# Kernel optimization log

Measured on AMD Instinct MI355X. Metric: run time of the kernel, lower is better.

The kernel has to match this reference:

```python
import jax, jax.numpy as jnp
import numpy as np

B, LAT, HC, HD, NB, S, E, NOTES = 64, 512, 1024, 1024, 16, 16, 128, 128
OUT = NOTES * 3  # 128 pitches x 3 states
L = 2            # num LSTM layers


def setup_inputs() -> dict:
    key = jax.random.key(0)
    ks = jax.random.split(key, 16)
    def w(k, *shape):
        return jax.random.normal(k, shape, jnp.float32) * 0.02
    G, GD = 4 * HC, 4 * HD
    z32 = lambda *s: jnp.zeros(s, jnp.float32)
    return {
        "z": jax.random.normal(ks[0], (B, LAT), jnp.float32),
        "target_pianoroll": jax.random.randint(ks[1], (B, NB * S, NOTES), 0, 3, jnp.int32),
        "w_zc": w(ks[2], HC * L * 2, LAT), "b_zc": z32(HC * L * 2),
        "c_wih0": w(ks[3], G, 1),  "c_whh0": w(ks[4], G, HC), "c_bih0": z32(G), "c_bhh0": z32(G),
        "c_wih1": w(ks[5], G, HC), "c_whh1": w(ks[6], G, HC), "c_bih1": z32(G), "c_bhh1": z32(G),
        "np_w": w(ks[7], E, NOTES), "np_b": z32(E),
        "cd_w": w(ks[8], HD * L * 2, HC), "cd_b": z32(HD * L * 2),
        "d_wih0": w(ks[9], GD, HC + E), "d_whh0": w(ks[10], GD, HD), "d_bih0": z32(GD), "d_bhh0": z32(GD),
        "d_wih1": w(ks[11], GD, HD),    "d_whh1": w(ks[12], GD, HD), "d_bih1": z32(GD), "d_bhh1": z32(GD),
        "op_w": w(ks[13], OUT, HD), "op_b": z32(OUT),
    }


def _lstm_cell(x, h, c, wih, whh, bih, bhh):
    g = x @ wih.T + h @ whh.T + (bih + bhh)
    i, f, gg, o = jnp.split(g, 4, axis=-1)  # PyTorch gate order i,f,g,o
    c = jax.nn.sigmoid(f) * c + jax.nn.sigmoid(i) * jnp.tanh(gg)
    h = jax.nn.sigmoid(o) * jnp.tanh(c)
    return h, c


def _run_lstm2(xs, h0, c0, p0, p1):
    # xs: [T, Bm, D]; h0/c0: [2, Bm, H]; returns [T, Bm, H] (top-layer outputs)
    def step(carry, xt):
        h0l, c0l, h1l, c1l = carry
        h0l, c0l = _lstm_cell(xt, h0l, c0l, *p0)
        h1l, c1l = _lstm_cell(h0l, h1l, c1l, *p1)
        return (h0l, c0l, h1l, c1l), h1l
    _, ys = jax.lax.scan(step, (h0[0], c0[0], h0[1], c0[1]), xs)
    return ys


def _forward(z, target_pianoroll, w_zc, b_zc,
             c_wih0, c_whh0, c_bih0, c_bhh0, c_wih1, c_whh1, c_bih1, c_bhh1,
             np_w, np_b, cd_w, cd_b,
             d_wih0, d_whh0, d_bih0, d_bhh0, d_wih1, d_whh1, d_bih1, d_bhh1,
             op_w, op_b):
    b = z.shape[0]
    # z -> conductor initial (h, c): view(B,2,L,HC).permute(2,0,3,1)
    ini = (z @ w_zc.T + b_zc).reshape(b, 2, L, HC)
    h_c0 = jnp.transpose(ini[:, 0], (1, 0, 2))  # [L, B, HC]
    c_c0 = jnp.transpose(ini[:, 1], (1, 0, 2))
    # Conductor LSTM over num_bars of zero inputs
    cond_xs = jnp.zeros((NB, b, 1), z.dtype)
    cond = _run_lstm2(cond_xs, h_c0, c_c0,
                      (c_wih0, c_whh0, c_bih0, c_bhh0),
                      (c_wih1, c_whh1, c_bih1, c_bhh1))  # [NB, B, HC]
    # Per-bar decoder initial states -> fold bars into batch ([L, NB*B, HD])
    di = (cond @ cd_w.T + cd_b).reshape(NB, b, 2, L, HD)
    h_d0 = jnp.transpose(di[:, :, 0], (2, 0, 1, 3)).reshape(L, NB * b, HD)
    c_d0 = jnp.transpose(di[:, :, 1], (2, 0, 1, 3)).reshape(L, NB * b, HD)
    # Teacher-forced prev inputs: zeros at t=0, shifted target otherwise
    tf = target_pianoroll.astype(z.dtype)                       # [B, NB*S, 128]
    prev = jnp.concatenate([jnp.zeros((b, 1, NOTES), z.dtype), tf[:, :-1]], axis=1)
    prev = jnp.transpose(prev.reshape(b, NB, S, NOTES), (2, 1, 0, 3)).reshape(S, NB * b, NOTES)
    emb = prev @ np_w.T + np_b                                   # [S, NB*B, E]
    bar = jnp.broadcast_to(cond.reshape(NB * b, HC), (S, NB * b, HC))
    xs = jnp.concatenate([emb, bar], axis=-1)                    # [S, NB*B, E+HC]
    ys = _run_lstm2(xs, h_d0, c_d0,
                    (d_wih0, d_whh0, d_bih0, d_bhh0),
                    (d_wih1, d_whh1, d_bih1, d_bhh1))            # [S, NB*B, HD]
    logits = ys @ op_w.T + op_b                                  # [S, NB*B, 384]
    logits = jnp.transpose(logits.reshape(S, NB, b, OUT), (2, 1, 0, 3))
    return logits.reshape(b, NB * S, NOTES, 3)


def reference(z, target_pianoroll, w_zc, b_zc,
              c_wih0, c_whh0, c_bih0, c_bhh0, c_wih1, c_whh1, c_bih1, c_bhh1,
              np_w, np_b, cd_w, cd_b,
              d_wih0, d_whh0, d_bih0, d_bhh0, d_wih1, d_whh1, d_bih1, d_bhh1,
              op_w, op_b):
    return _forward(z, target_pianoroll, w_zc, b_zc,
                    c_wih0, c_whh0, c_bih0, c_bhh0, c_wih1, c_whh1, c_bih1, c_bhh1,
                    np_w, np_b, cd_w, cd_b,
                    d_wih0, d_whh0, d_bih0, d_bhh0, d_wih1, d_whh1, d_bih1, d_bhh1,
                    op_w, op_b)
```

## Files before the change

### kernel.cpp

```cpp
#include <hip/hip_runtime.h>
#include <math.h>


typedef __attribute__((ext_vector_type(8))) short s16x8;
typedef __attribute__((ext_vector_type(8))) _Float16 f16x8;
typedef __attribute__((ext_vector_type(4))) float f32x4;

__device__ inline unsigned short f2h(float f) {
    _Float16 h = (_Float16)f;
    return __builtin_bit_cast(unsigned short, h);
}
__device__ inline float h2f(unsigned short u) {
    _Float16 h = __builtin_bit_cast(_Float16, u);
    return (float)h;
}

__device__ __forceinline__ void gload16(const unsigned short* g, char* l) {
    const unsigned int* gu = (const unsigned int*)g;
    unsigned int* lu = (unsigned int*)l;
    __builtin_amdgcn_global_load_lds(
        (const __attribute__((address_space(1))) unsigned int*)gu,
        (__attribute__((address_space(3))) unsigned int*)lu, 16, 0, 0);
}

__global__ __launch_bounds__(256) void gemm_mfma(
    int M, int N,
    const unsigned short* __restrict__ A1h, const unsigned short* __restrict__ A1l, int K1, int lda1,
    const unsigned short* __restrict__ W1h, int ldw1,
    const unsigned short* __restrict__ A2h, const unsigned short* __restrict__ A2l, int K2, int lda2,
    const unsigned short* __restrict__ W2h, int ldw2,
    const float* __restrict__ Add, int ldadd,
    const float* __restrict__ b1, const float* __restrict__ b2,
    float* __restrict__ C, int ldc,
    unsigned short* __restrict__ Chi, unsigned short* __restrict__ Clo,
    unsigned short* __restrict__ cpyh, unsigned short* __restrict__ cpyl,
    int mode, int scatter_s)
{
    __shared__ __align__(16) char ldsb[49152];

    const int tid = threadIdx.x;
    const int lane = tid & 63;
    const int wv = tid >> 6;
    const int wm = wv >> 1;
    const int wn = wv & 1;

    const int gx = gridDim.x;
    const int l = blockIdx.y * gx + blockIdx.x;
    const int nwg = gx * gridDim.y;
    const int l2 = (l & 7) * (nwg >> 3) + (l >> 3);
    const int bm = (l2 % gx) * 64;
    const int bn = (l2 / gx) * 128;

    const int j = (lane & 7) ^ (lane >> 3);
    const bool isLo = j >= 4;
    const int koff = (j & 3) * 8;
    const int rsub = lane >> 3;
    const int aR0 = bm + wv * 8 + rsub;
    const int brs = lane >> 2;
    const int j2 = (lane & 3) ^ ((lane >> 3) & 3);
    const int koffB = j2 * 8;

    f32x4 acc[2][4];
#pragma unroll
    for (int m = 0; m < 2; ++m)
#pragma unroll
        for (int n = 0; n < 4; ++n) acc[m][n] = (f32x4)0.0f;

    const int fr = lane & 15;
    const int kc = lane >> 4;

    const int NT = (K1 + K2) >> 5;

#define STAGE(dstp, t) {                                                        \
        const int k0_ = (t) << 5;                                               \
        const bool ph2_ = (k0_ >= K1);                                          \
        const unsigned short* Ab_ = ph2_ ? (isLo ? A2l : A2h)                   \
                                         : (isLo ? A1l : A1h);                  \
        const unsigned short* Wb_ = ph2_ ? W2h : W1h;                           \
        const int lda_ = ph2_ ? lda2 : lda1;                                    \
        const int ldw_ = ph2_ ? ldw2 : ldw1;                                    \
        const int kb_ = ph2_ ? (k0_ - K1) : k0_;                                \
        char* dst_ = (dstp);                                                    \
        gload16(Ab_ + (size_t)aR0 * lda_ + kb_ + koff,        dst_ + (wv    ) * 1024); \
        gload16(Ab_ + (size_t)(aR0 + 32) * lda_ + kb_ + koff, dst_ + (wv + 4) * 1024); \
        gload16(Wb_ + (size_t)(bn + wv * 16 + brs) * ldw_ + kb_ + koffB,        \
                dst_ + 8192 + wv * 1024);                                       \
        gload16(Wb_ + (size_t)(bn + 64 + wv * 16 + brs) * ldw_ + kb_ + koffB,   \
                dst_ + 8192 + 4096 + wv * 1024);                                \
    }

    char* bcur  = ldsb;
    char* bnext = ldsb + 16384;
    char* bfar  = ldsb + 32768;

    STAGE(bcur, 0);
    STAGE(bnext, 1);
    asm volatile("s_waitcnt vmcnt(4)" ::: "memory");
    __builtin_amdgcn_s_barrier();

    for (int t = 0; t < NT; ++t) {
        const bool more = (t + 2 < NT);
        if (more) STAGE(bfar, t + 2);
        {
            f16x8 ah[2], al[2], bh[4];
#pragma unroll
            for (int m = 0; m < 2; ++m) {
                const int row = wm * 32 + m * 16 + fr;
                const int sw = (row & 7) << 4;
                char* base = bcur + row * 128;
                ah[m] = *(const f16x8*)(base + ((kc * 16) ^ sw));
                al[m] = *(const f16x8*)(base + (((kc + 4) * 16) ^ sw));
            }
#pragma unroll
            for (int n = 0; n < 4; ++n) {
                const int brow = wn * 64 + n * 16 + fr;
                bh[n] = *(const f16x8*)(bcur + 8192 + brow * 64 +
                                        ((kc ^ ((brow >> 1) & 3)) << 4));
            }
            __builtin_amdgcn_s_setprio(1);
#pragma unroll
            for (int m = 0; m < 2; ++m)
#pragma unroll
                for (int n = 0; n < 4; ++n) {
                    acc[m][n] = __builtin_amdgcn_mfma_f32_16x16x32_f16(ah[m], bh[n], acc[m][n], 0, 0, 0);
                    acc[m][n] = __builtin_amdgcn_mfma_f32_16x16x32_f16(al[m], bh[n], acc[m][n], 0, 0, 0);
                }
            __builtin_amdgcn_s_setprio(0);
        }
        if (more) { asm volatile("s_waitcnt vmcnt(4)" ::: "memory"); }
        else      { asm volatile("s_waitcnt vmcnt(0)" ::: "memory"); }
        __builtin_amdgcn_s_barrier();
        char* tmp = bcur; bcur = bnext; bnext = bfar; bfar = tmp;
    }
#undef STAGE

    if (mode == 4) {
        float* ldsf = (float*)ldsb;
#pragma unroll
        for (int m = 0; m < 2; ++m)
#pragma unroll
            for (int n = 0; n < 4; ++n) {
                f32x4 v4 = acc[m][n];
#pragma unroll
                for (int q = 0; q < 4; ++q) {
                    const int rl = wm * 32 + m * 16 + kc * 4 + q;
                    const int cl = wn * 64 + n * 16 + fr;
                    const int col = bn + cl;
                    float v = v4[q];
                    if (b1) v += b1[col];
                    if (Add) v += Add[(size_t)(bm + rl) * ldadd + col];
                    ldsf[rl * 132 + cl] = v;
                }
            }
        __syncthreads();
        const int kb = bn >> 2;
#pragma unroll
        for (int e = 0; e < 8; ++e) {
            const int idx2 = tid * 8 + e;
            const int row = idx2 >> 5, kk = idx2 & 31;
            const float4 g4 = *(const float4*)(ldsf + row * 132 + kk * 4);
            const size_t ci = (((size_t)(bm + row)) << 10) + kb + kk;
            const float si = 1.f / (1.f + expf(-g4.x));
            const float sf = 1.f / (1.f + expf(-g4.y));
            const float so = 1.f / (1.f + expf(-g4.w));
            const float cn = sf * C[ci] + si * tanhf(g4.z);
            const float hn = so * tanhf(cn);
            C[ci] = cn;
            const unsigned short hh = f2h(hn);
            const unsigned short hl = f2h(hn - h2f(hh));
            Chi[ci] = hh; Clo[ci] = hl;
            if (cpyh) { cpyh[ci] = hh; cpyl[ci] = hl; }
        }
        return;
    }

#pragma unroll
    for (int m = 0; m < 2; ++m)
#pragma unroll
        for (int n = 0; n < 4; ++n) {
            f32x4 v4 = acc[m][n];
#pragma unroll
            for (int q = 0; q < 4; ++q) {
                const int rl = wm * 32 + m * 16 + kc * 4 + q;
                const int cl = wn * 64 + n * 16 + fr;
                const int r = bm + rl, col = bn + cl;
                float v = v4[q];
                if (b1) v += b1[col];
                if (b2) v += b2[col];
                if (Add) v += Add[(size_t)r * ldadd + col];
                if (mode == 0) {
                    C[(size_t)r * ldc + col] = v;
                } else if (mode == 1) {
                    unsigned short h = f2h(v);
                    Chi[(size_t)r * ldc + col] = h;
                    Clo[(size_t)r * ldc + col] = f2h(v - h2f(h));
                } else if (mode == 2) {
                    const int bb = r & 63, nb = r >> 6;
                    C[(size_t)(((bb * 16 + nb) * 16 + scatter_s)) * 384 + col] = v;
                } else {
                    const int bb = r & 63, nb = (r >> 6) & 15, s = r >> 10;
                    C[(size_t)(((bb * 16 + nb) * 16 + s)) * 384 + col] = v;
                }
            }
        }
}

__global__ __launch_bounds__(256) void gemm_mfma_n64(
    int M, int N,
    const unsigned short* __restrict__ A1h, const unsigned short* __restrict__ A1l, int K1, int lda1,
    const unsigned short* __restrict__ W1h, int ldw1,
    const unsigned short* __restrict__ A2h, const unsigned short* __restrict__ A2l, int K2, int lda2,
    const unsigned short* __restrict__ W2h, int ldw2,
    const float* __restrict__ b1,
    float* __restrict__ C, int ldc,
    unsigned short* __restrict__ Chi, unsigned short* __restrict__ Clo,
    unsigned short* __restrict__ cpyh, unsigned short* __restrict__ cpyl,
    int mode)
{
    __shared__ __align__(16) char ldsb[36864];

    const int tid = threadIdx.x;
    const int lane = tid & 63;
    const int wv = tid >> 6;

    const int gx = gridDim.x;
    const int l = blockIdx.y * gx + blockIdx.x;
    const int nwg = gx * gridDim.y;
    const int l2 = (l & 7) * (nwg >> 3) + (l >> 3);
    const int bm = (l2 % gx) * 64;
    const int bn = (l2 / gx) * 64;

    const int j = (lane & 7) ^ (lane >> 3);
    const bool isLo = j >= 4;
    const int koff = (j & 3) * 8;
    const int rsub = lane >> 3;
    const int aR0 = bm + wv * 8 + rsub;
    const int brs = lane >> 2;
    const int j2 = (lane & 3) ^ ((lane >> 3) & 3);
    const int koffB = j2 * 8;

    f32x4 acc[4];
#pragma unroll
    for (int m = 0; m < 4; ++m) acc[m] = (f32x4)0.0f;

    const int fr = lane & 15;
    const int kc = lane >> 4;

    const int NT = (K1 + K2) >> 5;

#define STAGE64(dstp, t) {                                                      \
        const int k0_ = (t) << 5;                                               \
        const bool ph2_ = (k0_ >= K1);                                          \
        const unsigned short* Ab_ = ph2_ ? (isLo ? A2l : A2h)                   \
                                         : (isLo ? A1l : A1h);                  \
        const unsigned short* Wb_ = ph2_ ? W2h : W1h;                           \
        const int lda_ = ph2_ ? lda2 : lda1;                                    \
        const int ldw_ = ph2_ ? ldw2 : ldw1;                                    \
        const int kb_ = ph2_ ? (k0_ - K1) : k0_;                                \
        char* dst_ = (dstp);                                                    \
        gload16(Ab_ + (size_t)aR0 * lda_ + kb_ + koff,        dst_ + (wv    ) * 1024); \
        gload16(Ab_ + (size_t)(aR0 + 32) * lda_ + kb_ + koff, dst_ + (wv + 4) * 1024); \
        gload16(Wb_ + (size_t)(bn + wv * 16 + brs) * ldw_ + kb_ + koffB,        \
                dst_ + 8192 + wv * 1024);                                       \
    }

    char* bcur  = ldsb;
    char* bnext = ldsb + 12288;
    char* bfar  = ldsb + 24576;

    STAGE64(bcur, 0);
    STAGE64(bnext, 1);
    asm volatile("s_waitcnt vmcnt(3)" ::: "memory");
    __builtin_amdgcn_s_barrier();

    for (int t = 0; t < NT; ++t) {
        const bool more = (t + 2 < NT);
        if (more) STAGE64(bfar, t + 2);
        {
            f16x8 ah[4], al[4], bh;
#pragma unroll
            for (int m = 0; m < 4; ++m) {
                const int row = m * 16 + fr;
                const int sw = (row & 7) << 4;
                char* base = bcur + row * 128;
                ah[m] = *(const f16x8*)(base + ((kc * 16) ^ sw));
                al[m] = *(const f16x8*)(base + (((kc + 4) * 16) ^ sw));
            }
            {
                const int brow = wv * 16 + fr;
                bh = *(const f16x8*)(bcur + 8192 + brow * 64 +
                                     ((kc ^ ((brow >> 1) & 3)) << 4));
            }
            __builtin_amdgcn_s_setprio(1);
#pragma unroll
            for (int m = 0; m < 4; ++m) {
                acc[m] = __builtin_amdgcn_mfma_f32_16x16x32_f16(ah[m], bh, acc[m], 0, 0, 0);
                acc[m] = __builtin_amdgcn_mfma_f32_16x16x32_f16(al[m], bh, acc[m], 0, 0, 0);
            }
            __builtin_amdgcn_s_setprio(0);
        }
        if (more) { asm volatile("s_waitcnt vmcnt(3)" ::: "memory"); }
        else      { asm volatile("s_waitcnt vmcnt(0)" ::: "memory"); }
        __builtin_amdgcn_s_barrier();
        char* tmp = bcur; bcur = bnext; bnext = bfar; bfar = tmp;
    }
#undef STAGE64

    if (mode == 4) {
        float* ldsf = (float*)ldsb;
#pragma unroll
        for (int m = 0; m < 4; ++m) {
            f32x4 v4 = acc[m];
#pragma unroll
            for (int q = 0; q < 4; ++q) {
                const int rl = m * 16 + kc * 4 + q;
                const int cl = wv * 16 + fr;
                float v = v4[q];
                if (b1) v += b1[bn + cl];
                ldsf[rl * 68 + cl] = v;
            }
        }
        __syncthreads();
        const int kb = bn >> 2;
#pragma unroll
        for (int e = 0; e < 4; ++e) {
            const int idx2 = tid * 4 + e;
            const int row = idx2 >> 4, kk = idx2 & 15;
            const float4 g4 = *(const float4*)(ldsf + row * 68 + kk * 4);
            const size_t ci = (((size_t)(bm + row)) << 10) + kb + kk;
            const float si = 1.f / (1.f + expf(-g4.x));
            const float sf = 1.f / (1.f + expf(-g4.y));
            const float so = 1.f / (1.f + expf(-g4.w));
            const float cn = sf * C[ci] + si * tanhf(g4.z);
            const float hn = so * tanhf(cn);
            C[ci] = cn;
            const unsigned short hh = f2h(hn);
            const unsigned short hl = f2h(hn - h2f(hh));
            Chi[ci] = hh; Clo[ci] = hl;
            if (cpyh) { cpyh[ci] = hh; cpyl[ci] = hl; }
        }
        return;
    }

#pragma unroll
    for (int m = 0; m < 4; ++m) {
        f32x4 v4 = acc[m];
#pragma unroll
        for (int q = 0; q < 4; ++q) {
            const int rl = m * 16 + kc * 4 + q;
            const int cl = wv * 16 + fr;
            const int r = bm + rl, col = bn + cl;
            float v = v4[q];
            if (b1) v += b1[col];
            C[(size_t)r * ldc + col] = v;
        }
    }
}

__global__ __launch_bounds__(256) void split_pack(
    const float* __restrict__ src, int ldsrc, int c0, long total, int C,
    unsigned short* __restrict__ hi, unsigned short* __restrict__ lo)
{
    long i = ((long)blockIdx.x * 256 + threadIdx.x) * 4;
    if (i >= total) return;
    int r = (int)(i / C), c = (int)(i % C);
    float4 v = *(const float4*)(src + (size_t)r * ldsrc + c0 + c);
#pragma unroll
    for (int j = 0; j < 4; ++j) {
        float x = (&v.x)[j];
        unsigned short h = f2h(x);
        hi[i + j] = h;
        lo[i + j] = f2h(x - h2f(h));
    }
}

__global__ __launch_bounds__(256) void split_pack_perm(
    const float* __restrict__ src, int ldsrc, int c0, long total, int C,
    unsigned short* __restrict__ hi, unsigned short* __restrict__ lo)
{
    long i = ((long)blockIdx.x * 256 + threadIdx.x) * 4;
    if (i >= total) return;
    int r = (int)(i / C), c = (int)(i % C);
    int sr = (r & 3) * 1024 + (r >> 2);
    float4 v = *(const float4*)(src + (size_t)sr * ldsrc + c0 + c);
#pragma unroll
    for (int j = 0; j < 4; ++j) {
        float x = (&v.x)[j];
        unsigned short h = f2h(x);
        hi[i + j] = h;
        lo[i + j] = f2h(x - h2f(h));
    }
}

__global__ __launch_bounds__(256) void bias_perm(
    const float* __restrict__ a, const float* __restrict__ b, float* __restrict__ dst)
{
    const int j = blockIdx.x * 256 + threadIdx.x;
    if (j >= 4096) return;
    const int o = (j & 3) * 1024 + (j >> 2);
    dst[j] = a[o] + b[o];
}

__global__ __launch_bounds__(256) void scatter_ini_split(
    const float* __restrict__ I, unsigned short* __restrict__ hchi,
    unsigned short* __restrict__ hclo, float* __restrict__ cc)
{
    const int idx = blockIdx.x * blockDim.x + threadIdx.x;
    if (idx >= 131072) return;
    const int k = idx & 1023, b = (idx >> 10) & 63, l = idx >> 16;
    const float* row = I + (size_t)b * 4096;
    float hv = row[(l << 10) + k];
    unsigned short h = f2h(hv);
    hchi[idx] = h; hclo[idx] = f2h(hv - h2f(h));
    cc[idx] = row[2048 + (l << 10) + k];
}

__global__ __launch_bounds__(256) void scatter_di_split(
    const float* __restrict__ D,
    unsigned short* __restrict__ h0h, unsigned short* __restrict__ h0l,
    unsigned short* __restrict__ h1h, unsigned short* __restrict__ h1l,
    float* __restrict__ cd0, float* __restrict__ cd1)
{
    const int idx = blockIdx.x * blockDim.x + threadIdx.x;
    if (idx >= 1048576) return;
    const int k = idx & 1023, r = idx >> 10;
    const float* row = D + ((size_t)r << 12);
    float v0 = row[k], v1 = row[1024 + k];
    unsigned short a = f2h(v0); h0h[idx] = a; h0l[idx] = f2h(v0 - h2f(a));
    unsigned short b = f2h(v1); h1h[idx] = b; h1l[idx] = f2h(v1 - h2f(b));
    cd0[idx] = row[2048 + k];
    cd1[idx] = row[3072 + k];
}

__global__ __launch_bounds__(256) void build_prev_b(
    const int* __restrict__ tp, unsigned short* __restrict__ ph, unsigned short* __restrict__ pl)
{
    const int idx = blockIdx.x * blockDim.x + threadIdx.x;
    if (idx >= 2097152) return;
    const int n = idx & 127;
    const int r = (idx >> 7) & 1023;
    const int s = idx >> 17;
    const int nb = r >> 6, bb = r & 63;
    const int t = nb * 16 + s;
    float v = 0.f;
    if (t > 0) v = (float)tp[(size_t)bb * 32768 + (size_t)(t - 1) * 128 + n];
    ph[idx] = f2h(v);
    pl[idx] = 0;
}

#define BM 64
#define BN 64
#define BK 16

__global__ __launch_bounds__(256) void gemm_f32(
    int M, int N,
    const float* __restrict__ A1, int K1, int lda1,
    const float* __restrict__ W1, int ldw1,
    const float* __restrict__ A2, int K2, int lda2,
    const float* __restrict__ W2, int ldw2,
    const float* __restrict__ Add, int ldadd,
    const float* __restrict__ bias1, const float* __restrict__ bias2,
    float* __restrict__ C, int ldc, int scatter_s)
{
    __shared__ float As[BK][BM];
    __shared__ float Ws[BK][BN];
    const int bm = blockIdx.x * BM;
    const int bn = blockIdx.y * BN;
    const int tid = threadIdx.x;
    const int ty = tid >> 4;
    const int tx = tid & 15;
    const int lr = tid >> 2;
    const int lc = (tid & 3) << 2;

    float acc[4][4] = {{0.f,0.f,0.f,0.f},{0.f,0.f,0.f,0.f},{0.f,0.f,0.f,0.f},{0.f,0.f,0.f,0.f}};

    for (int phase = 0; phase < 2; ++phase) {
        const float* Ap = phase ? A2 : A1;
        const float* Wp = phase ? W2 : W1;
        const int K   = phase ? K2 : K1;
        const int lda = phase ? lda2 : lda1;
        const int ldw = phase ? ldw2 : ldw1;
        if (Ap == nullptr || K <= 0) continue;
        for (int k0 = 0; k0 < K; k0 += BK) {
            float4 av = *(const float4*)(Ap + (size_t)(bm + lr) * lda + k0 + lc);
            float4 wv = *(const float4*)(Wp + (size_t)(bn + lr) * ldw + k0 + lc);
            __syncthreads();
            As[lc+0][lr] = av.x; As[lc+1][lr] = av.y; As[lc+2][lr] = av.z; As[lc+3][lr] = av.w;
            Ws[lc+0][lr] = wv.x; Ws[lc+1][lr] = wv.y; Ws[lc+2][lr] = wv.z; Ws[lc+3][lr] = wv.w;
            __syncthreads();
            #pragma unroll
            for (int k = 0; k < BK; ++k) {
                float4 a = *(const float4*)&As[k][ty << 2];
                float4 w = *(const float4*)&Ws[k][tx << 2];
                acc[0][0] = fmaf(a.x, w.x, acc[0][0]);
                acc[0][1] = fmaf(a.x, w.y, acc[0][1]);
                acc[0][2] = fmaf(a.x, w.z, acc[0][2]);
                acc[0][3] = fmaf(a.x, w.w, acc[0][3]);
                acc[1][0] = fmaf(a.y, w.x, acc[1][0]);
                acc[1][1] = fmaf(a.y, w.y, acc[1][1]);
                acc[1][2] = fmaf(a.y, w.z, acc[1][2]);
                acc[1][3] = fmaf(a.y, w.w, acc[1][3]);
                acc[2][0] = fmaf(a.z, w.x, acc[2][0]);
                acc[2][1] = fmaf(a.z, w.y, acc[2][1]);
                acc[2][2] = fmaf(a.z, w.z, acc[2][2]);
                acc[2][3] = fmaf(a.z, w.w, acc[2][3]);
                acc[3][0] = fmaf(a.w, w.x, acc[3][0]);
                acc[3][1] = fmaf(a.w, w.y, acc[3][1]);
                acc[3][2] = fmaf(a.w, w.z, acc[3][2]);
                acc[3][3] = fmaf(a.w, w.w, acc[3][3]);
            }
        }
    }

    #pragma unroll
    for (int i = 0; i < 4; ++i) {
        const int row = bm + (ty << 2) + i;
        #pragma unroll
        for (int j = 0; j < 4; ++j) {
            const int col = bn + (tx << 2) + j;
            float v = acc[i][j];
            if (bias1) v += bias1[col];
            if (bias2) v += bias2[col];
            if (Add)   v += Add[(size_t)row * ldadd + col];
            if (scatter_s >= 0) {
                const int bb = row & 63, nb = row >> 6;
                C[(size_t)(((bb * 16 + nb) * 16 + scatter_s)) * 384 + col] = v;
            } else {
                C[(size_t)row * ldc + col] = v;
            }
        }
    }
}

__global__ __launch_bounds__(256) void lstm_cell(
    const float* __restrict__ g, float* __restrict__ c,
    float* __restrict__ h, float* __restrict__ hcopy, int M)
{
    const int idx = blockIdx.x * blockDim.x + threadIdx.x;
    if (idx >= (M << 10)) return;
    const int r = idx >> 10, k = idx & 1023;
    const float* gr = g + ((size_t)r << 12);
    const float gi = gr[k], gf = gr[k + 1024], gg = gr[k + 2048], go = gr[k + 3072];
    const float si = 1.f / (1.f + expf(-gi));
    const float sf = 1.f / (1.f + expf(-gf));
    const float so = 1.f / (1.f + expf(-go));
    const float cn = sf * c[idx] + si * tanhf(gg);
    const float hn = so * tanhf(cn);
    c[idx] = cn;
    h[idx] = hn;
    if (hcopy) hcopy[idx] = hn;
}

__global__ __launch_bounds__(256) void scatter_ini(
    const float* __restrict__ I, float* __restrict__ hc, float* __restrict__ cc)
{
    const int idx = blockIdx.x * blockDim.x + threadIdx.x;
    if (idx >= 131072) return;
    const int k = idx & 1023, b = (idx >> 10) & 63, l = idx >> 16;
    const float* row = I + (size_t)b * 4096;
    hc[idx] = row[(l << 10) + k];
    cc[idx] = row[2048 + (l << 10) + k];
}

__global__ __launch_bounds__(256) void scatter_di(
    const float* __restrict__ D, float* __restrict__ hd0, float* __restrict__ cd0,
    float* __restrict__ hd1, float* __restrict__ cd1)
{
    const int idx = blockIdx.x * blockDim.x + threadIdx.x;
    if (idx >= 1048576) return;
    const int k = idx & 1023, r = idx >> 10;
    const float* row = D + ((size_t)r << 12);
    hd0[idx] = row[k];
    hd1[idx] = row[1024 + k];
    cd0[idx] = row[2048 + k];
    cd1[idx] = row[3072 + k];
}

__global__ __launch_bounds__(256) void build_prev(
    const int* __restrict__ tp, float* __restrict__ prevf)
{
    const int idx = blockIdx.x * blockDim.x + threadIdx.x;
    if (idx >= 2097152) return;
    const int n = idx & 127;
    const int r = (idx >> 7) & 1023;
    const int s = idx >> 17;
    const int nb = r >> 6, bb = r & 63;
    const int t = nb * 16 + s;
    float v = 0.f;
    if (t > 0) v = (float)tp[(size_t)bb * 32768 + (size_t)(t - 1) * 128 + n];
    prevf[idx] = v;
}

extern "C" void kernel_launch(void* const* d_in, const int* in_sizes, int n_in,
                              void* d_out, int out_size, void* d_ws, size_t ws_size,
                              hipStream_t stream)
{
    (void)in_sizes; (void)n_in; (void)out_size;
    const float* z      = (const float*)d_in[0];
    const int*   tp     = (const int*)  d_in[1];
    const float* w_zc   = (const float*)d_in[2];
    const float* b_zc   = (const float*)d_in[3];
    const float* c_whh0 = (const float*)d_in[5];
    const float* c_bih0 = (const float*)d_in[6];
    const float* c_bhh0 = (const float*)d_in[7];
    const float* c_wih1 = (const float*)d_in[8];
    const float* c_whh1 = (const float*)d_in[9];
    const float* c_bih1 = (const float*)d_in[10];
    const float* c_bhh1 = (const float*)d_in[11];
    const float* np_w   = (const float*)d_in[12];
    const float* np_b   = (const float*)d_in[13];
    const float* cd_w   = (const float*)d_in[14];
    const float* cd_b   = (const float*)d_in[15];
    const float* d_wih0 = (const float*)d_in[16];
    const float* d_whh0 = (const float*)d_in[17];
    const float* d_bih0 = (const float*)d_in[18];
    const float* d_bhh0 = (const float*)d_in[19];
    const float* d_wih1 = (const float*)d_in[20];
    const float* d_whh1 = (const float*)d_in[21];
    const float* d_bih1 = (const float*)d_in[22];
    const float* d_bhh1 = (const float*)d_in[23];
    const float* op_w   = (const float*)d_in[24];
    const float* op_b   = (const float*)d_in[25];
    float* out = (float*)d_out;

    size_t o = 0;
    auto alloc = [&](size_t bytes) { size_t r = o; o = (o + bytes + 255) & ~(size_t)255; return r; };
    const size_t oCW0 = alloc((size_t)4096*1024*4);
    const size_t oCW1 = alloc((size_t)4096*1024*4);
    const size_t oCW2 = alloc((size_t)4096*1024*4);
    const size_t oWZC = alloc((size_t)4096*512*4);
    const size_t oNPW = alloc((size_t)128*128*4);
    const size_t oZS  = alloc((size_t)64*512*4);
    const size_t oCDW = alloc((size_t)4096*1024*4);
    const size_t oD0R = alloc((size_t)4096*1024*4);
    const size_t oCG  = alloc((size_t)64*4096*4);
    const size_t oCC  = alloc((size_t)2*64*1024*4);
    const size_t oHCa = alloc((size_t)2*64*1024*4);
    const size_t oHCb = alloc((size_t)2*64*1024*4);
    const size_t oCND = alloc((size_t)1024*1024*4);
    const size_t oEMB = alloc((size_t)16*1024*128*4);
    const size_t oBRP = alloc((size_t)1024*4096*4);
    const size_t oDG  = alloc((size_t)1024*4096*4);
    const size_t oHD0a= alloc((size_t)1024*1024*4);
    const size_t oHD0b= alloc((size_t)1024*1024*4);
    const size_t oHD1a= alloc((size_t)1024*1024*4);
    const size_t oHD1b= alloc((size_t)1024*1024*4);
    const size_t oCD0 = alloc((size_t)1024*1024*4);
    const size_t oCD1 = alloc((size_t)1024*1024*4);
    const size_t oBS  = alloc((size_t)4*4096*4);
    const size_t need = o;
    const size_t oH1S = alloc((size_t)16*1024*1024*4);
    const size_t need_batched = o;

    if (ws_size >= need) {
        const bool batched = (ws_size >= need_batched);
        char* ws = (char*)d_ws;
        unsigned short* CW0 = (unsigned short*)(ws + oCW0);
        unsigned short* CW1 = (unsigned short*)(ws + oCW1);
        unsigned short* CW2 = (unsigned short*)(ws + oCW2);
        unsigned short* WZC = (unsigned short*)(ws + oWZC);
        unsigned short* NPW = (unsigned short*)(ws + oNPW);
        unsigned short* ZS  = (unsigned short*)(ws + oZS);
        unsigned short* CDW = (unsigned short*)(ws + oCDW);
        unsigned short* D0R = (unsigned short*)(ws + oD0R);
        float* CG  = (float*)(ws + oCG);
        float* CC  = (float*)(ws + oCC);
        unsigned short* HCa = (unsigned short*)(ws + oHCa);
        unsigned short* HCb = (unsigned short*)(ws + oHCb);
        unsigned short* CND = (unsigned short*)(ws + oCND);
        unsigned short* PRV = (unsigned short*)(ws + oDG);
        unsigned short* EMB = (unsigned short*)(ws + oEMB);
        float* BRP = (float*)(ws + oBRP);
        float* DG  = (float*)(ws + oDG);
        unsigned short* HD0a = (unsigned short*)(ws + oHD0a);
        unsigned short* HD0b = (unsigned short*)(ws + oHD0b);
        unsigned short* HD1a = (unsigned short*)(ws + oHD1a);
        unsigned short* HD1b = (unsigned short*)(ws + oHD1b);
        float* CD0 = (float*)(ws + oCD0);
        float* CD1 = (float*)(ws + oCD1);
        float* BSC0 = (float*)(ws + oBS);
        float* BSC1 = BSC0 + 4096;
        float* BSB0 = BSC1 + 4096;
        float* BSD1 = BSB0 + 4096;
        unsigned short* H1S  = (unsigned short*)(ws + oH1S);
        unsigned short* H1Sl = H1S + (size_t)16*1048576;
        unsigned short* DWHH0 = CW0;
        unsigned short* DWIH1 = CW1;
        unsigned short* DWHH1 = CW2;
        unsigned short* D0E   = WZC;
        unsigned short* OPW   = WZC + (size_t)2*4096*128;

        auto split = [&](const float* src, int ldsrc, int c0, long R, long C, unsigned short* dst) {
            long total = R * C;
            split_pack<<<(unsigned)((total/4 + 255) / 256), 256, 0, stream>>>(
                src, ldsrc, c0, total, (int)C, dst, dst + total);
        };
        auto splitP = [&](const float* src, int ldsrc, int c0, long C, unsigned short* dst) {
            long total = 4096 * C;
            split_pack_perm<<<(unsigned)((total/4 + 255) / 256), 256, 0, stream>>>(
                src, ldsrc, c0, total, (int)C, dst, dst + total);
        };
        auto gemm2 = [&](int M, int N,
                         const unsigned short* A1h, const unsigned short* A1l, int K1, int lda1,
                         const unsigned short* W1, int ldw1,
                         const unsigned short* A2h, const unsigned short* A2l, int K2, int lda2,
                         const unsigned short* W2, int ldw2,
                         const float* Addp, int ldadd, const float* bb1, const float* bb2,
                         float* Cp, int ldc, unsigned short* Chi, unsigned short* Clo,
                         unsigned short* cpyh, unsigned short* cpyl,
                         int mode, int ss) {
            dim3 grid(M / 64, N / 128);
            gemm_mfma<<<grid, 256, 0, stream>>>(M, N, A1h, A1l, K1, lda1, W1, ldw1,
                                                A2h, A2l, K2, lda2, W2, ldw2,
                                                Addp, ldadd, bb1, bb2, Cp, ldc, Chi, Clo,
                                                cpyh, cpyl, mode, ss);
        };
        auto gemmN64 = [&](int M, int N,
                           const unsigned short* A1h, const unsigned short* A1l, int K1, int lda1,
                           const unsigned short* W1, int ldw1,
                           const unsigned short* A2h, const unsigned short* A2l, int K2, int lda2,
                           const unsigned short* W2, int ldw2,
                           const float* bb1, float* Cp, int ldc,
                           unsigned short* Chi, unsigned short* Clo,
                           unsigned short* cpyh, unsigned short* cpyl, int mode) {
            dim3 grid(M / 64, N / 64);
            gemm_mfma_n64<<<grid, 256, 0, stream>>>(M, N, A1h, A1l, K1, lda1, W1, ldw1,
                                                    A2h, A2l, K2, lda2, W2, ldw2,
                                                    bb1, Cp, ldc, Chi, Clo, cpyh, cpyl, mode);
        };

        auto hc0h = [&](int b){ return (b ? HCb : HCa); };
        auto hc0l = [&](int b){ return (b ? HCb : HCa) + 131072; };
        auto hc1h = [&](int b){ return (b ? HCb : HCa) + 65536; };
        auto hc1l = [&](int b){ return (b ? HCb : HCa) + 131072 + 65536; };
        auto hd0h = [&](int b){ return (b ? HD0b : HD0a); };
        auto hd0l = [&](int b){ return (b ? HD0b : HD0a) + 1048576; };
        auto hd1h = [&](int b){ return (b ? HD1b : HD1a); };
        auto hd1l = [&](int b){ return (b ? HD1b : HD1a) + 1048576; };

        split(z, 512, 0, 64, 512, ZS);
        split(w_zc, 512, 0, 4096, 512, WZC);
        splitP(c_whh0, 1024, 0, 1024, CW0);
        splitP(c_wih1, 1024, 0, 1024, CW1);
        splitP(c_whh1, 1024, 0, 1024, CW2);
        split(np_w, 128, 0, 128, 128, NPW);
        split(cd_w, 1024, 0, 4096, 1024, CDW);
        splitP(d_wih0, 1152, 128, 1024, D0R);
        bias_perm<<<16, 256, 0, stream>>>(c_bih0, c_bhh0, BSC0);
        bias_perm<<<16, 256, 0, stream>>>(c_bih1, c_bhh1, BSC1);
        bias_perm<<<16, 256, 0, stream>>>(d_bih0, d_bhh0, BSB0);
        bias_perm<<<16, 256, 0, stream>>>(d_bih1, d_bhh1, BSD1);
        build_prev_b<<<8192, 256, 0, stream>>>(tp, PRV, PRV + 2097152);

        gemmN64(64, 4096, ZS, ZS + 32768, 512, 512, WZC, 512,
                nullptr, nullptr, 0, 0, nullptr, 0,
                b_zc, CG, 4096, nullptr, nullptr, nullptr, nullptr, 0);
        scatter_ini_split<<<512, 256, 0, stream>>>(CG, HCa, HCa + 131072, CC);

        gemm2(16384, 128, PRV, PRV + 2097152, 128, 128, NPW, 128,
              nullptr, nullptr, 0, 0, nullptr, 0,
              nullptr, 0, np_b, nullptr, nullptr, 128, EMB, EMB + 2097152, nullptr, nullptr, 1, -1);

        for (int t = 0; t < 16; ++t) {
            const int p = t & 1;
            gemmN64(64, 4096, hc0h(p), hc0l(p), 1024, 1024, CW0, 1024,
                    nullptr, nullptr, 0, 0, nullptr, 0,
                    BSC0, CC, 0, hc0h(p ^ 1), hc0l(p ^ 1), nullptr, nullptr, 4);
            gemmN64(64, 4096, hc0h(p ^ 1), hc0l(p ^ 1), 1024, 1024, CW1, 1024,
                    hc1h(p), hc1l(p), 1024, 1024, CW2, 1024,
                    BSC1, CC + 65536, 0, hc1h(p ^ 1), hc1l(p ^ 1),
                    CND + t * 65536, CND + 1048576 + t * 65536, 4);
        }

        splitP(d_whh0, 1024, 0, 1024, DWHH0);
        splitP(d_wih1, 1024, 0, 1024, DWIH1);
        splitP(d_whh1, 1024, 0, 1024, DWHH1);
        splitP(d_wih0, 1152, 0, 128, D0E);
        split(op_w, 1024, 0, 384, 1024, OPW);

        gemm2(1024, 4096, CND, CND + 1048576, 1024, 1024, CDW, 1024,
              nullptr, nullptr, 0, 0, nullptr, 0,
              nullptr, 0, cd_b, nullptr, DG, 4096, nullptr, nullptr, nullptr, nullptr, 0, -1);
        scatter_di_split<<<4096, 256, 0, stream>>>(DG, HD0a, HD0a + 1048576,
                                                   HD1a, HD1a + 1048576, CD0, CD1);

        gemm2(1024, 4096, CND, CND + 1048576, 1024, 1024, D0R, 1024,
              nullptr, nullptr, 0, 0, nullptr, 0,
              nullptr, 0, BSB0, nullptr, BRP, 4096, nullptr, nullptr, nullptr, nullptr, 0, -1);

        for (int s = 0; s < 16; ++s) {
            const int p = s & 1;
            gemm2(1024, 4096, EMB + (size_t)s * 131072, EMB + 2097152 + (size_t)s * 131072, 128, 128,
                  D0E, 128,
                  hd0h(p), hd0l(p), 1024, 1024, DWHH0, 1024,
                  BRP, 4096, nullptr, nullptr, CD0, 0, hd0h(p ^ 1), hd0l(p ^ 1),
                  nullptr, nullptr, 4, -1);
            gemm2(1024, 4096, hd0h(p ^ 1), hd0l(p ^ 1), 1024, 1024, DWIH1, 1024,
                  hd1h(p), hd1l(p), 1024, 1024, DWHH1, 1024,
                  nullptr, 0, BSD1, nullptr, CD1, 0, hd1h(p ^ 1), hd1l(p ^ 1),
                  batched ? H1S + (size_t)s * 1048576 : nullptr,
                  batched ? H1Sl + (size_t)s * 1048576 : nullptr, 4, -1);
            if (!batched) {
                gemm2(1024, 384, hd1h(p ^ 1), hd1l(p ^ 1), 1024, 1024, OPW, 1024,
                      nullptr, nullptr, 0, 0, nullptr, 0,
                      nullptr, 0, op_b, nullptr, out, 384, nullptr, nullptr, nullptr, nullptr, 2, s);
            }
        }
        if (batched) {
            gemm2(16384, 384, H1S, H1Sl, 1024, 1024, OPW, 1024,
                  nullptr, nullptr, 0, 0, nullptr, 0,
                  nullptr, 0, op_b, nullptr, out, 384, nullptr, nullptr, nullptr, nullptr, 3, -1);
        }
        return;
    }

    float* wsf     = (float*)d_ws;
    float* hc      = wsf;
    float* cc      = hc + 131072;
    float* cond    = cc + 131072;
    float* cg      = cond + 1048576;
    float* barpart = cg + 262144;
    float* emb     = barpart + 4194304;
    float* prevf   = emb + 2097152;
    float* hd0     = prevf + 2097152;
    float* cd0     = hd0 + 1048576;
    float* hd1     = cd0 + 1048576;
    float* cd1     = hd1 + 1048576;
    float* dg      = cd1 + 1048576;

    auto gemmf = [&](int M, int N,
                     const float* A1, int K1, int lda1, const float* W1, int ldw1,
                     const float* A2, int K2, int lda2, const float* W2, int ldw2,
                     const float* Addp, int ldadd, const float* bb1, const float* bb2,
                     float* Cp, int ldc, int ss) {
        dim3 grid(M / BM, N / BN);
        gemm_f32<<<grid, dim3(256), 0, stream>>>(M, N, A1, K1, lda1, W1, ldw1,
                                                 A2, K2, lda2, W2, ldw2,
                                                 Addp, ldadd, bb1, bb2, Cp, ldc, ss);
    };

    gemmf(64, 4096, z, 512, 512, w_zc, 512, nullptr, 0, 0, nullptr, 0,
          nullptr, 0, b_zc, nullptr, cg, 4096, -1);
    scatter_ini<<<512, 256, 0, stream>>>(cg, hc, cc);

    build_prev<<<8192, 256, 0, stream>>>(tp, prevf);
    gemmf(16384, 128, prevf, 128, 128, np_w, 128, nullptr, 0, 0, nullptr, 0,
          nullptr, 0, np_b, nullptr, emb, 128, -1);

    for (int t = 0; t < 16; ++t) {
        gemmf(64, 4096, hc, 1024, 1024, c_whh0, 1024, nullptr, 0, 0, nullptr, 0,
              nullptr, 0, c_bih0, c_bhh0, cg, 4096, -1);
        lstm_cell<<<256, 256, 0, stream>>>(cg, cc, hc, nullptr, 64);
        gemmf(64, 4096, hc, 1024, 1024, c_wih1, 1024,
              hc + 65536, 1024, 1024, c_whh1, 1024,
              nullptr, 0, c_bih1, c_bhh1, cg, 4096, -1);
        lstm_cell<<<256, 256, 0, stream>>>(cg, cc + 65536, hc + 65536, cond + t * 65536, 64);
    }

    gemmf(1024, 4096, cond, 1024, 1024, cd_w, 1024, nullptr, 0, 0, nullptr, 0,
          nullptr, 0, cd_b, nullptr, dg, 4096, -1);
    scatter_di<<<4096, 256, 0, stream>>>(dg, hd0, cd0, hd1, cd1);

    gemmf(1024, 4096, cond, 1024, 1024, d_wih0 + 128, 1152, nullptr, 0, 0, nullptr, 0,
          nullptr, 0, d_bih0, d_bhh0, barpart, 4096, -1);

    for (int s = 0; s < 16; ++s) {
        gemmf(1024, 4096, emb + (size_t)s * 131072, 128, 128, d_wih0, 1152,
              hd0, 1024, 1024, d_whh0, 1024,
              barpart, 4096, nullptr, nullptr, dg, 4096, -1);
        lstm_cell<<<4096, 256, 0, stream>>>(dg, cd0, hd0, nullptr, 1024);
        gemmf(1024, 4096, hd0, 1024, 1024, d_wih1, 1024,
              hd1, 1024, 1024, d_whh1, 1024,
              nullptr, 0, d_bih1, d_bhh1, dg, 4096, -1);
        lstm_cell<<<4096, 256, 0, stream>>>(dg, cd1, hd1, nullptr, 1024);
        gemmf(1024, 384, hd1, 1024, 1024, op_w, 1024, nullptr, 0, 0, nullptr, 0,
              nullptr, 0, op_b, nullptr, out, 384, s);
    }
}
```

Baseline: 2.440 ms.

## Switch GEMM to double-buffered 64-wide K steps with one barrier per step

Replaces the triple-buffered 32-wide K pipeline with a double-buffered pipeline that stages two 32-wide K slices per iteration into 64KB of LDS. Each iteration computes both slices, which halves the number of barriers and waits per K. The trade-off is higher LDS use, which may reduce occupancy, and a shallower prefetch with a full vmcnt(0) wait. It also assumes K1+K2 is a multiple of 64 and that K1 is aligned so the phase switch still falls on 32-element boundaries.

Result: no change. 2.423 ms (-0.7%).

```diff
diff --git a/kernel.cpp b/kernel.cpp
--- a/kernel.cpp
+++ b/kernel.cpp
@@ -36,7 +36,7 @@
     unsigned short* __restrict__ cpyh, unsigned short* __restrict__ cpyl,
     int mode, int scatter_s)
 {
-    __shared__ __align__(16) char ldsb[49152];
+    __shared__ __align__(16) char ldsb[65536];
 
     const int tid = threadIdx.x;
     const int lane = tid & 63;
@@ -69,10 +69,10 @@
     const int fr = lane & 15;
     const int kc = lane >> 4;
 
-    const int NT = (K1 + K2) >> 5;
-
-#define STAGE(dstp, t) {                                                        \
-        const int k0_ = (t) << 5;                                               \
+    const int NT = (K1 + K2) >> 6;
+
+#define STAGE(dstp, kt) {                                                       \
+        const int k0_ = (kt) << 5;                                              \
         const bool ph2_ = (k0_ >= K1);                                          \
         const unsigned short* Ab_ = ph2_ ? (isLo ? A2l : A2h)                   \
                                          : (isLo ? A1l : A1h);                  \
@@ -89,50 +89,56 @@
                 dst_ + 8192 + 4096 + wv * 1024);                                \
     }
 
+#define COMPUTE32(sb) {                                                         \
+        char* sbp = (sb);                                                       \
+        f16x8 ah[2], al[2], bh[4];                                              \
+        _Pragma("unroll")                                                       \
+        for (int m = 0; m < 2; ++m) {                                           \
+            const int row = wm * 32 + m * 16 + fr;                              \
+            const int sw = (row & 7) << 4;                                      \
+            char* base = sbp + row * 128;                                       \
+            ah[m] = *(const f16x8*)(base + ((kc * 16) ^ sw));                   \
+            al[m] = *(const f16x8*)(base + (((kc + 4) * 16) ^ sw));             \
+        }                                                                       \
+        _Pragma("unroll")                                                       \
+        for (int n = 0; n < 4; ++n) {                                           \
+            const int brow = wn * 64 + n * 16 + fr;                             \
+            bh[n] = *(const f16x8*)(sbp + 8192 + brow * 64 +                    \
+                                    ((kc ^ ((brow >> 1) & 3)) << 4));           \
+        }                                                                       \
+        __builtin_amdgcn_s_setprio(1);                                          \
+        _Pragma("unroll")                                                       \
+        for (int m = 0; m < 2; ++m)                                             \
+            _Pragma("unroll")                                                   \
+            for (int n = 0; n < 4; ++n) {                                       \
+                acc[m][n] = __builtin_amdgcn_mfma_f32_16x16x32_f16(ah[m], bh[n], acc[m][n], 0, 0, 0); \
+                acc[m][n] = __builtin_amdgcn_mfma_f32_16x16x32_f16(al[m], bh[n], acc[m][n], 0, 0, 0); \
+            }                                                                   \
+        __builtin_amdgcn_s_setprio(0);                                          \
+    }
+
     char* bcur  = ldsb;
-    char* bnext = ldsb + 16384;
-    char* bfar  = ldsb + 32768;
+    char* bnext = ldsb + 32768;
 
     STAGE(bcur, 0);
-    STAGE(bnext, 1);
-    asm volatile("s_waitcnt vmcnt(4)" ::: "memory");
+    STAGE(bcur + 16384, 1);
+    asm volatile("s_waitcnt vmcnt(0)" ::: "memory");
     __builtin_amdgcn_s_barrier();
 
     for (int t = 0; t < NT; ++t) {
-        const bool more = (t + 2 < NT);
-        if (more) STAGE(bfar, t + 2);
-        {
-            f16x8 ah[2], al[2], bh[4];
-#pragma unroll
-            for (int m = 0; m < 2; ++m) {
-                const int row = wm * 32 + m * 16 + fr;
-                const int sw = (row & 7) << 4;
-                char* base = bcur + row * 128;
-                ah[m] = *(const f16x8*)(base + ((kc * 16) ^ sw));
-                al[m] = *(const f16x8*)(base + (((kc + 4) * 16) ^ sw));
-            }
-#pragma unroll
-            for (int n = 0; n < 4; ++n) {
-                const int brow = wn * 64 + n * 16 + fr;
-                bh[n] = *(const f16x8*)(bcur + 8192 + brow * 64 +
-                                        ((kc ^ ((brow >> 1) & 3)) << 4));
-            }
-            __builtin_amdgcn_s_setprio(1);
-#pragma unroll
-            for (int m = 0; m < 2; ++m)
-#pragma unroll
-                for (int n = 0; n < 4; ++n) {
-                    acc[m][n] = __builtin_amdgcn_mfma_f32_16x16x32_f16(ah[m], bh[n], acc[m][n], 0, 0, 0);
-                    acc[m][n] = __builtin_amdgcn_mfma_f32_16x16x32_f16(al[m], bh[n], acc[m][n], 0, 0, 0);
-                }
-            __builtin_amdgcn_s_setprio(0);
-        }
-        if (more) { asm volatile("s_waitcnt vmcnt(4)" ::: "memory"); }
-        else      { asm volatile("s_waitcnt vmcnt(0)" ::: "memory"); }
+        const bool more = (t + 1 < NT);
+        if (more) {
+            STAGE(bnext, 2 * (t + 1));
+            STAGE(bnext + 16384, 2 * (t + 1) + 1);
+        }
+        COMPUTE32(bcur);
+        COMPUTE32(bcur + 16384);
+        asm volatile("s_waitcnt vmcnt(0)" ::: "memory");
         __builtin_amdgcn_s_barrier();
-        char* tmp = bcur; bcur = bnext; bnext = bfar; bfar = tmp;
+        char* tmp = bcur; bcur = bnext; bnext = tmp;
     }
 #undef STAGE
+#undef COMPUTE32
 
     if (mode == 4) {
         float* ldsf = (float*)ldsb;
```
